# Performance work log

Measured on AMD Instinct MI355X. Metric: run time of the kernel, lower is better.

## Reference

```python
import jax, jax.numpy as jnp
import numpy as np

N_NODES = 100000
N_EDGES = 1600000
D_IN = 128
D_OUT = 128
KEEP_PROB = 0.5  # torch code: p_drop = 1 - self.dropout, dropout=0.5


def setup_inputs() -> dict:
    key = jax.random.key(0)
    k1, k2, k3, k4, k5 = jax.random.split(key, 5)
    x = jax.random.normal(k1, (N_NODES, D_IN), dtype=jnp.float32)
    # Glorot uniform init matching weight_variable_glorot
    init_range = np.sqrt(6.0 / (D_IN + D_OUT))
    W = jax.random.uniform(k2, (D_IN, D_OUT), dtype=jnp.float32,
                           minval=-init_range, maxval=init_range)
    adj_row = jax.random.randint(k3, (N_EDGES,), 0, N_NODES, dtype=jnp.int32)
    adj_col = jax.random.randint(k4, (N_EDGES,), 0, N_NODES, dtype=jnp.int32)
    adj_val = jax.random.uniform(k5, (N_EDGES,), dtype=jnp.float32)
    return {"x": x, "W": W, "adj_row": adj_row, "adj_col": adj_col, "adj_val": adj_val}


def reference(x, W, adj_row, adj_col, adj_val):
    # dropout (always training=True in the torch module), deterministic key
    mask = jax.random.bernoulli(jax.random.key(42), KEEP_PROB, x.shape)
    x = jnp.where(mask, x / KEEP_PROB, 0.0)
    # dense GEMM: [N, D_in] @ [D_in, D_out]
    h = x @ W
    # sparse adjacency SpMM in COO form: out[r] += val * h[c]
    msg = adj_val[:, None] * h[adj_col]            # [E, D_out]
    agg = jax.ops.segment_sum(msg, adj_row, num_segments=N_NODES)
    return jax.nn.relu(agg)
```

## Files before the change

### kernel.cpp

```cpp
#include <hip/hip_runtime.h>
#include <hip/hip_bf16.h>

#define N_NODES 100000
#define N_EDGES 1600000
#define D 128
#define NC 391
#define CCAP 5120
#define NF 3125
#define C1S 32
#define RSS 257
#define GCAP 1024
#define GEMM_H1 1563
#define GEMM_H2 1562

typedef float          floatx4 __attribute__((ext_vector_type(4)));
typedef __bf16         bf16x8  __attribute__((ext_vector_type(8)));
typedef unsigned short ushort8 __attribute__((ext_vector_type(8)));

__device__ __forceinline__ unsigned rotl32(unsigned x, int d) {
    return (x << d) | (x >> (32 - d));
}

__device__ __forceinline__ void threefry_0_42(unsigned c0, unsigned c1,
                                              unsigned& o0, unsigned& o1) {
    const unsigned k0 = 0u, k1 = 42u;
    const unsigned k2 = 0x1BD11BDAu ^ k0 ^ k1;
    unsigned x0 = c0 + k0;
    unsigned x1 = c1 + k1;
#define TF_R4(r0, r1, r2, r3)                      \
    x0 += x1; x1 = rotl32(x1, r0); x1 ^= x0;       \
    x0 += x1; x1 = rotl32(x1, r1); x1 ^= x0;       \
    x0 += x1; x1 = rotl32(x1, r2); x1 ^= x0;       \
    x0 += x1; x1 = rotl32(x1, r3); x1 ^= x0;
    TF_R4(13, 15, 26, 6);  x0 += k1; x1 += k2 + 1u;
    TF_R4(17, 29, 16, 24); x0 += k2; x1 += k0 + 2u;
    TF_R4(13, 15, 26, 6);  x0 += k0; x1 += k1 + 3u;
    TF_R4(17, 29, 16, 24); x0 += k1; x1 += k2 + 4u;
    TF_R4(13, 15, 26, 6);  x0 += k2; x1 += k0 + 5u;
#undef TF_R4
    o0 = x0; o1 = x1;
}

__device__ __forceinline__ bool keep_elem(unsigned i) {
    unsigned o0, o1;
    threefry_0_42(0u, i, o0, o1);
    return (((o0 ^ o1) >> 31) == 0u);
}

__device__ __forceinline__ unsigned short f32_bf16(float f) {
    unsigned u = __float_as_uint(f);
    u += 0x7fffu + ((u >> 16) & 1u);
    return (unsigned short)(u >> 16);
}

__device__ __forceinline__ void gemm_body(const float* __restrict__ x,
                                          const float* __restrict__ W,
                                          unsigned short* __restrict__ hb,
                                          unsigned short (*Wt)[136],
                                          unsigned short (*xs)[136],
                                          int g, int t) {
    {
        int n      = t & 127;
        int k8base = t >> 7;
#pragma unroll
        for (int it = 0; it < 8; ++it) {
            int k8 = (it * 2 + k8base) * 8;
            unsigned short tmp[8];
#pragma unroll
            for (int j = 0; j < 8; ++j)
                tmp[j] = f32_bf16(W[(k8 + j) * 128 + n]);
            *(ushort8*)&Wt[n][k8] = *(ushort8*)tmp;
        }
    }
    {
        int m  = t >> 4;
        int c0 = (t & 15) * 8;
        int r0 = g * 32 + m;
        const float* pa = x + r0 * D + c0;
        const float* pb = x + (r0 + 16) * D + c0;
        float va[8], vb[8];
        *(float4*)&va[0] = ((const float4*)pa)[0];
        *(float4*)&va[4] = ((const float4*)pa)[1];
        *(float4*)&vb[0] = ((const float4*)pb)[0];
        *(float4*)&vb[4] = ((const float4*)pb)[1];
        int ibase = r0 * D + c0;
        unsigned short ta[8], tb[8];
#pragma unroll
        for (int j = 0; j < 8; ++j) {
            float fa = keep_elem((unsigned)(ibase + j))        ? 2.0f * va[j] : 0.0f;
            float fb = keep_elem((unsigned)(ibase + 2048 + j)) ? 2.0f * vb[j] : 0.0f;
            ta[j] = f32_bf16(fa);
            tb[j] = f32_bf16(fb);
        }
        *(ushort8*)&xs[m][c0]      = *(ushort8*)ta;
        *(ushort8*)&xs[16 + m][c0] = *(ushort8*)tb;
    }
    __syncthreads();

    const int w  = t >> 6;
    const int l  = t & 63;
    const int rt = w >> 1;
    const int ctbase = (w & 1) * 4;
    const int mm = l & 15;
    const int q  = l >> 4;
    const int koff = q * 8;
    const unsigned short* xrow = &xs[rt * 16 + mm][0];
    const int growbase = g * 32 + rt * 16;

    for (int ci = 0; ci < 4; ++ci) {
        int ct = ctbase + ci;
        const unsigned short* wrow = &Wt[ct * 16 + mm][0];
        floatx4 acc = {0.f, 0.f, 0.f, 0.f};
#pragma unroll
        for (int kt = 0; kt < 4; ++kt) {
            bf16x8 a = *(const bf16x8*)(xrow + kt * 32 + koff);
            bf16x8 b = *(const bf16x8*)(wrow + kt * 32 + koff);
            acc = __builtin_amdgcn_mfma_f32_16x16x32_bf16(a, b, acc, 0, 0, 0);
        }
        int col = ct * 16 + mm;
#pragma unroll
        for (int reg = 0; reg < 4; ++reg) {
            int grow = growbase + q * 4 + reg;
            hb[grow * D + col] = f32_bf16(acc[reg]);
        }
    }
}

__global__ __launch_bounds__(256)
void k_p1(const float* __restrict__ x, const float* __restrict__ W,
          unsigned short* __restrict__ hb,
          const int* __restrict__ row, const int* __restrict__ col,
          const float* __restrict__ val, int* __restrict__ cnt1,
          int2* __restrict__ buf) {
    __shared__ __align__(16) unsigned short Wt[128][136];
    __shared__ __align__(16) unsigned short xs[32][136];
    __shared__ int h[NC];
    __shared__ int lbase[NC];

    const int t = threadIdx.x;
    if (blockIdx.x >= NC) {
        gemm_body(x, W, hb, Wt, xs, blockIdx.x - NC, t);
        return;
    }

    for (int i = t; i < NC; i += 256) h[i] = 0;
    __syncthreads();

    int rows[16], cols[16];
    float vals[16];
    int base = blockIdx.x * 4096;
#pragma unroll
    for (int k = 0; k < 4; ++k) {
        int e4 = base + (k * 256 + t) * 4;
        if (e4 < N_EDGES) {
            *(int4*)&rows[k * 4]   = *(const int4*)(row + e4);
            *(int4*)&cols[k * 4]   = *(const int4*)(col + e4);
            *(float4*)&vals[k * 4] = *(const float4*)(val + e4);
        } else {
            rows[k * 4] = rows[k * 4 + 1] = rows[k * 4 + 2] = rows[k * 4 + 3] = -1;
        }
    }
#pragma unroll
    for (int j = 0; j < 16; ++j)
        if (rows[j] >= 0) atomicAdd(&h[rows[j] >> 8], 1);
    __syncthreads();

    for (int i = t; i < NC; i += 256) {
        int c = h[i];
        lbase[i] = c ? atomicAdd(&cnt1[i * C1S], c) : 0;
    }
    __syncthreads();
    for (int i = t; i < NC; i += 256) h[i] = 0;
    __syncthreads();

#pragma unroll
    for (int j = 0; j < 16; ++j) {
        if (rows[j] >= 0) {
            int bb  = rows[j] >> 8;
            int pos = lbase[bb] + atomicAdd(&h[bb], 1);
            if (pos < CCAP) {
                int2 ent;
                ent.x = (cols[j] << 7) | ((rows[j] & 255) << 24);
                ent.y = __float_as_int(vals[j]);
                buf[bb * CCAP + pos] = ent;
            }
        }
    }
}

__global__ __launch_bounds__(256)
void k_p2(const float* __restrict__ x, const float* __restrict__ W,
          unsigned short* __restrict__ hb,
          const int* __restrict__ cnt1, int2* __restrict__ buf,
          int* __restrict__ rs) {
    __shared__ __align__(16) unsigned short Wt[128][136];
    __shared__ __align__(16) unsigned short xs[32][136];
    __shared__ int h[4][256];
    __shared__ int wsum[4];

    const int t = threadIdx.x;
    if (blockIdx.x >= NC) {
        gemm_body(x, W, hb, Wt, xs, blockIdx.x - NC + GEMM_H1, t);
        return;
    }

    const int c = blockIdx.x;
    const int w = t >> 6;
    int n = cnt1[c * C1S];
    if (n > CCAP) n = CCAP;
    int2* slab = buf + c * CCAP;

    for (int i = t; i < 1024; i += 256) ((int*)h)[i] = 0;
    __syncthreads();

    int2 er[20];
#pragma unroll
    for (int k = 0; k < 20; ++k) {
        int i = k * 256 + t;
        if (i < n) {
            er[k] = slab[i];
            atomicAdd(&h[w][((unsigned)er[k].x) >> 24], 1);
        }
    }
    __syncthreads();

    int v = h[0][t] + h[1][t] + h[2][t] + h[3][t];
    int xsc = v;
#pragma unroll
    for (int off = 1; off < 64; off <<= 1) {
        int u = __shfl_up(xsc, off);
        if ((t & 63) >= off) xsc += u;
    }
    if ((t & 63) == 63) wsum[t >> 6] = xsc;
    __syncthreads();
    int wo = 0;
    for (int k = 0; k < (t >> 6); ++k) wo += wsum[k];
    int basex = xsc - v + wo;
    rs[c * RSS + t] = basex;
    if (t == 0) rs[c * RSS + 256] = n;
    int s = basex;
#pragma unroll
    for (int wv = 0; wv < 4; ++wv) {
        int tmp = h[wv][t];
        h[wv][t] = s;
        s += tmp;
    }
    __syncthreads();

#pragma unroll
    for (int k = 0; k < 20; ++k) {
        int i = k * 256 + t;
        if (i < n) {
            int pos = atomicAdd(&h[w][((unsigned)er[k].x) >> 24], 1);
            slab[pos] = er[k];
        }
    }
}

__global__ __launch_bounds__(256, 8)
void k_gather(const int* __restrict__ rs, const int2* __restrict__ buf,
              const unsigned short* __restrict__ hb, float* __restrict__ out) {
    __shared__ __align__(16) int2 eL[GCAP];

    const int b = blockIdx.x, t = threadIdx.x;
    const int c = b >> 3;
    const int2* slab = buf + c * CCAP;
    const int* rsb = rs + c * RSS + (b & 7) * 32;
    const int rs0 = rsb[0];
    int nf = rsb[32] - rs0;
    if (nf > GCAP) nf = GCAP;

    for (int i = t; i < nf; i += 256) eL[i] = slab[rs0 + i];
    __syncthreads();

    const int w  = t >> 6;
    const int l2 = (t & 63) * 2;
    const unsigned short* hbl = hb + l2;
    for (int r = 0; r < 8; ++r) {
        int rl = w * 8 + r;
        int s0 = rsb[rl] - rs0;
        int e0 = rsb[rl + 1] - rs0;
        if (e0 > nf) e0 = nf;
        int cc = e0 - s0;
        float a0 = 0.f, a1 = 0.f;
        int i = 0;
        for (; i + 16 <= cc; i += 16) {
            unsigned ex[16];
            float    vv[16];
#pragma unroll
            for (int j = 0; j < 16; ++j) {
                int2 e = eL[s0 + i + j];
                ex[j] = (unsigned)e.x & 0xFFFFFFu;
                vv[j] = __int_as_float(e.y);
            }
            unsigned hv[16];
#pragma unroll
            for (int j = 0; j < 16; ++j)
                hv[j] = *(const unsigned*)(hbl + ex[j]);
#pragma unroll
            for (int j = 0; j < 16; ++j) {
                a0 = fmaf(vv[j], __uint_as_float(hv[j] << 16), a0);
                a1 = fmaf(vv[j], __uint_as_float(hv[j] & 0xffff0000u), a1);
            }
        }
        for (; i + 4 <= cc; i += 4) {
            unsigned ex[4];
            float    vv[4];
#pragma unroll
            for (int j = 0; j < 4; ++j) {
                int2 e = eL[s0 + i + j];
                ex[j] = (unsigned)e.x & 0xFFFFFFu;
                vv[j] = __int_as_float(e.y);
            }
            unsigned hv[4];
#pragma unroll
            for (int j = 0; j < 4; ++j)
                hv[j] = *(const unsigned*)(hbl + ex[j]);
#pragma unroll
            for (int j = 0; j < 4; ++j) {
                a0 = fmaf(vv[j], __uint_as_float(hv[j] << 16), a0);
                a1 = fmaf(vv[j], __uint_as_float(hv[j] & 0xffff0000u), a1);
            }
        }
        for (; i < cc; ++i) {
            int2 e = eL[s0 + i];
            float v = __int_as_float(e.y);
            unsigned hv = *(const unsigned*)(hbl + ((unsigned)e.x & 0xFFFFFFu));
            a0 = fmaf(v, __uint_as_float(hv << 16), a0);
            a1 = fmaf(v, __uint_as_float(hv & 0xffff0000u), a1);
        }
        int grow = (b << 5) + rl;
        float2 rr;
        rr.x = a0 > 0.f ? a0 : 0.f;
        rr.y = a1 > 0.f ? a1 : 0.f;
        *(float2*)(out + grow * D + l2) = rr;
    }
}

extern "C" void kernel_launch(void* const* d_in, const int* in_sizes, int n_in,
                              void* d_out, int out_size, void* d_ws, size_t ws_size,
                              hipStream_t stream) {
    const float* x    = (const float*)d_in[0];
    const float* W    = (const float*)d_in[1];
    const int*   arow = (const int*)d_in[2];
    const int*   acol = (const int*)d_in[3];
    const float* aval = (const float*)d_in[4];
    float* out = (float*)d_out;

    char* ws = (char*)d_ws;
    unsigned short* hb = (unsigned short*)ws;
    size_t off = 25600000;
    int* cnt1 = (int*)(ws + off); off += NC * C1S * 4;
    off = (off + 127) & ~(size_t)127;
    int* rs   = (int*)(ws + off); off += NC * RSS * 4;
    off = (off + 127) & ~(size_t)127;
    int2* buf = (int2*)(ws + off); off += (size_t)NC * CCAP * 8;

    hipMemsetAsync(cnt1, 0, NC * C1S * 4, stream);
    k_p1     <<<NC + GEMM_H1, 256, 0, stream>>>(x, W, hb, arow, acol, aval, cnt1, buf);
    k_p2     <<<NC + GEMM_H2, 256, 0, stream>>>(x, W, hb, cnt1, buf, rs);
    k_gather <<<NF, 256, 0, stream>>>(rs, buf, hb, out);
}
```

Before: 222.5 us.

## Pre-pack W into MFMA fragments, drop per-block W LDS staging, flatten gather loop

A small prep kernel converts W once to bf16 in MFMA fragment order and also zeroes the counters, which replaces the memset. GEMM blocks then load their W fragments straight into registers instead of each block transposing all of W into LDS. This removes a large LDS allocation and redundant per-block conversion work. The gather kernel now walks each wave's whole edge range in one loop and flushes on row-id changes, which avoids per-row loop overhead and uneven unrolling on short rows. Occupancy hints are also changed: 4 for p1/p2, and 8 down to 6 for gather.

```diff
diff --git a/kernel.cpp b/kernel.cpp
--- a/kernel.cpp
+++ b/kernel.cpp
@@ -53,25 +53,37 @@
     return (unsigned short)(u >> 16);
 }
 
+__global__ __launch_bounds__(256)
+void k_wprep(const float* __restrict__ W, unsigned short* __restrict__ Wf,
+             int* __restrict__ cnt1) {
+    int g = blockIdx.x * 256 + threadIdx.x;
+    for (int i = g; i < NC * C1S; i += 2048) cnt1[i] = 0;
+    int combo = g >> 6, l = g & 63;
+    int ct = combo >> 2, kt = combo & 3;
+    int mm = l & 15, q = l >> 4;
+    unsigned short tmp[8];
+#pragma unroll
+    for (int j = 0; j < 8; ++j)
+        tmp[j] = f32_bf16(W[(kt * 32 + q * 8 + j) * 128 + ct * 16 + mm]);
+    *(ushort8*)&Wf[g * 8] = *(ushort8*)tmp;
+}
+
 __device__ __forceinline__ void gemm_body(const float* __restrict__ x,
-                                          const float* __restrict__ W,
+                                          const unsigned short* __restrict__ Wf,
                                           unsigned short* __restrict__ hb,
-                                          unsigned short (*Wt)[136],
                                           unsigned short (*xs)[136],
                                           int g, int t) {
-    {
-        int n      = t & 127;
-        int k8base = t >> 7;
-#pragma unroll
-        for (int it = 0; it < 8; ++it) {
-            int k8 = (it * 2 + k8base) * 8;
-            unsigned short tmp[8];
-#pragma unroll
-            for (int j = 0; j < 8; ++j)
-                tmp[j] = f32_bf16(W[(k8 + j) * 128 + n]);
-            *(ushort8*)&Wt[n][k8] = *(ushort8*)tmp;
-        }
-    }
+    const int w = t >> 6, l = t & 63;
+    const int rt = w >> 1, ctbase = (w & 1) * 4;
+    const int mm = l & 15, q = l >> 4, koff = q * 8;
+
+    bf16x8 wf[4][4];
+#pragma unroll
+    for (int ci = 0; ci < 4; ++ci)
+#pragma unroll
+        for (int kt = 0; kt < 4; ++kt)
+            wf[ci][kt] = *(const bf16x8*)&Wf[(((ctbase + ci) * 4 + kt) * 64 + l) * 8];
+
     {
         int m  = t >> 4;
         int c0 = (t & 15) * 8;
@@ -97,27 +109,20 @@
     }
     __syncthreads();
 
-    const int w  = t >> 6;
-    const int l  = t & 63;
-    const int rt = w >> 1;
-    const int ctbase = (w & 1) * 4;
-    const int mm = l & 15;
-    const int q  = l >> 4;
-    const int koff = q * 8;
     const unsigned short* xrow = &xs[rt * 16 + mm][0];
+    bf16x8 af[4];
+#pragma unroll
+    for (int kt = 0; kt < 4; ++kt)
+        af[kt] = *(const bf16x8*)(xrow + kt * 32 + koff);
+
     const int growbase = g * 32 + rt * 16;
-
+#pragma unroll
     for (int ci = 0; ci < 4; ++ci) {
-        int ct = ctbase + ci;
-        const unsigned short* wrow = &Wt[ct * 16 + mm][0];
         floatx4 acc = {0.f, 0.f, 0.f, 0.f};
 #pragma unroll
-        for (int kt = 0; kt < 4; ++kt) {
-            bf16x8 a = *(const bf16x8*)(xrow + kt * 32 + koff);
-            bf16x8 b = *(const bf16x8*)(wrow + kt * 32 + koff);
-            acc = __builtin_amdgcn_mfma_f32_16x16x32_bf16(a, b, acc, 0, 0, 0);
-        }
-        int col = ct * 16 + mm;
+        for (int kt = 0; kt < 4; ++kt)
+            acc = __builtin_amdgcn_mfma_f32_16x16x32_bf16(af[kt], wf[ci][kt], acc, 0, 0, 0);
+        int col = (ctbase + ci) * 16 + mm;
 #pragma unroll
         for (int reg = 0; reg < 4; ++reg) {
             int grow = growbase + q * 4 + reg;
@@ -126,20 +131,19 @@
     }
 }
 
-__global__ __launch_bounds__(256)
-void k_p1(const float* __restrict__ x, const float* __restrict__ W,
+__global__ __launch_bounds__(256, 4)
+void k_p1(const float* __restrict__ x, const unsigned short* __restrict__ Wf,
           unsigned short* __restrict__ hb,
           const int* __restrict__ row, const int* __restrict__ col,
           const float* __restrict__ val, int* __restrict__ cnt1,
           int2* __restrict__ buf) {
-    __shared__ __align__(16) unsigned short Wt[128][136];
     __shared__ __align__(16) unsigned short xs[32][136];
     __shared__ int h[NC];
     __shared__ int lbase[NC];
 
     const int t = threadIdx.x;
     if (blockIdx.x >= NC) {
-        gemm_body(x, W, hb, Wt, xs, blockIdx.x - NC, t);
+        gemm_body(x, Wf, hb, xs, blockIdx.x - NC, t);
         return;
     }
 
@@ -188,19 +192,18 @@
     }
 }
 
-__global__ __launch_bounds__(256)
-void k_p2(const float* __restrict__ x, const float* __restrict__ W,
+__global__ __launch_bounds__(256, 4)
+void k_p2(const float* __restrict__ x, const unsigned short* __restrict__ Wf,
           unsigned short* __restrict__ hb,
           const int* __restrict__ cnt1, int2* __restrict__ buf,
           int* __restrict__ rs) {
-    __shared__ __align__(16) unsigned short Wt[128][136];
     __shared__ __align__(16) unsigned short xs[32][136];
     __shared__ int h[4][256];
     __shared__ int wsum[4];
 
     const int t = threadIdx.x;
     if (blockIdx.x >= NC) {
-        gemm_body(x, W, hb, Wt, xs, blockIdx.x - NC + GEMM_H1, t);
+        gemm_body(x, Wf, hb, xs, blockIdx.x - NC + GEMM_H1, t);
         return;
     }
 
@@ -257,7 +260,7 @@
     }
 }
 
-__global__ __launch_bounds__(256, 8)
+__global__ __launch_bounds__(256, 6)
 void k_gather(const int* __restrict__ rs, const int2* __restrict__ buf,
               const unsigned short* __restrict__ hb, float* __restrict__ out) {
     __shared__ __align__(16) int2 eL[GCAP];
@@ -276,65 +279,76 @@
     const int w  = t >> 6;
     const int l2 = (t & 63) * 2;
     const unsigned short* hbl = hb + l2;
-    for (int r = 0; r < 8; ++r) {
-        int rl = w * 8 + r;
-        int s0 = rsb[rl] - rs0;
-        int e0 = rsb[rl + 1] - rs0;
-        if (e0 > nf) e0 = nf;
-        int cc = e0 - s0;
-        float a0 = 0.f, a1 = 0.f;
-        int i = 0;
-        for (; i + 16 <= cc; i += 16) {
-            unsigned ex[16];
-            float    vv[16];
-#pragma unroll
-            for (int j = 0; j < 16; ++j) {
-                int2 e = eL[s0 + i + j];
-                ex[j] = (unsigned)e.x & 0xFFFFFFu;
-                vv[j] = __int_as_float(e.y);
-            }
-            unsigned hv[16];
-#pragma unroll
-            for (int j = 0; j < 16; ++j)
-                hv[j] = *(const unsigned*)(hbl + ex[j]);
-#pragma unroll
-            for (int j = 0; j < 16; ++j) {
-                a0 = fmaf(vv[j], __uint_as_float(hv[j] << 16), a0);
-                a1 = fmaf(vv[j], __uint_as_float(hv[j] & 0xffff0000u), a1);
-            }
-        }
-        for (; i + 4 <= cc; i += 4) {
-            unsigned ex[4];
-            float    vv[4];
-#pragma unroll
-            for (int j = 0; j < 4; ++j) {
-                int2 e = eL[s0 + i + j];
-                ex[j] = (unsigned)e.x & 0xFFFFFFu;
-                vv[j] = __int_as_float(e.y);
-            }
-            unsigned hv[4];
-#pragma unroll
-            for (int j = 0; j < 4; ++j)
-                hv[j] = *(const unsigned*)(hbl + ex[j]);
-#pragma unroll
-            for (int j = 0; j < 4; ++j) {
-                a0 = fmaf(vv[j], __uint_as_float(hv[j] << 16), a0);
-                a1 = fmaf(vv[j], __uint_as_float(hv[j] & 0xffff0000u), a1);
-            }
-        }
-        for (; i < cc; ++i) {
-            int2 e = eL[s0 + i];
-            float v = __int_as_float(e.y);
-            unsigned hv = *(const unsigned*)(hbl + ((unsigned)e.x & 0xFFFFFFu));
-            a0 = fmaf(v, __uint_as_float(hv << 16), a0);
-            a1 = fmaf(v, __uint_as_float(hv & 0xffff0000u), a1);
-        }
-        int grow = (b << 5) + rl;
-        float2 rr;
-        rr.x = a0 > 0.f ? a0 : 0.f;
-        rr.y = a1 > 0.f ? a1 : 0.f;
-        *(float2*)(out + grow * D + l2) = rr;
-    }
+
+    int s0w = rsb[w * 8] - rs0;     if (s0w > nf) s0w = nf;
+    int e0w = rsb[w * 8 + 8] - rs0; if (e0w > nf) e0w = nf;
+
+    float a0 = 0.f, a1 = 0.f;
+    int cur = w * 8;
+    const int wtop = w * 8 + 8;
+
+#define STORE_ROW(R, X0, X1)                                      \
+    {                                                             \
+        float2 rr;                                                \
+        rr.x = (X0) > 0.f ? (X0) : 0.f;                           \
+        rr.y = (X1) > 0.f ? (X1) : 0.f;                           \
+        *(float2*)(out + ((b << 5) + (R)) * D + l2) = rr;         \
+    }
+#define FLUSH(RID)                                                \
+    if ((RID) != cur) {                                           \
+        STORE_ROW(cur, a0, a1);                                   \
+        for (int z = cur + 1; z < (RID); ++z) STORE_ROW(z, 0.f, 0.f); \
+        a0 = 0.f; a1 = 0.f; cur = (RID);                          \
+    }
+
+    int i = s0w;
+    for (; i + 16 <= e0w; i += 16) {
+        int2 e[16];
+#pragma unroll
+        for (int j = 0; j < 16; ++j) e[j] = eL[i + j];
+        unsigned hv[16];
+#pragma unroll
+        for (int j = 0; j < 16; ++j)
+            hv[j] = *(const unsigned*)(hbl + ((unsigned)e[j].x & 0xFFFFFFu));
+#pragma unroll
+        for (int j = 0; j < 16; ++j) {
+            int rid = ((unsigned)e[j].x >> 24) & 31;
+            FLUSH(rid);
+            float v = __int_as_float(e[j].y);
+            a0 = fmaf(v, __uint_as_float(hv[j] << 16), a0);
+            a1 = fmaf(v, __uint_as_float(hv[j] & 0xffff0000u), a1);
+        }
+    }
+    for (; i + 4 <= e0w; i += 4) {
+        int2 e[4];
+#pragma unroll
+        for (int j = 0; j < 4; ++j) e[j] = eL[i + j];
+        unsigned hv[4];
+#pragma unroll
+        for (int j = 0; j < 4; ++j)
+            hv[j] = *(const unsigned*)(hbl + ((unsigned)e[j].x & 0xFFFFFFu));
+#pragma unroll
+        for (int j = 0; j < 4; ++j) {
+            int rid = ((unsigned)e[j].x >> 24) & 31;
+            FLUSH(rid);
+            float v = __int_as_float(e[j].y);
+            a0 = fmaf(v, __uint_as_float(hv[j] << 16), a0);
+            a1 = fmaf(v, __uint_as_float(hv[j] & 0xffff0000u), a1);
+        }
+    }
+    for (; i < e0w; ++i) {
+        int2 e = eL[i];
+        unsigned hv = *(const unsigned*)(hbl + ((unsigned)e.x & 0xFFFFFFu));
+        int rid = ((unsigned)e.x >> 24) & 31;
+        FLUSH(rid);
+        float v = __int_as_float(e.y);
+        a0 = fmaf(v, __uint_as_float(hv << 16), a0);
+        a1 = fmaf(v, __uint_as_float(hv & 0xffff0000u), a1);
+    }
+    STORE_ROW(cur, a0, a1);
+    for (int z = cur + 1; z < wtop; ++z) STORE_ROW(z, 0.f, 0.f);
+#undef FLUSH
+#undef STORE_ROW
 }
 
 extern "C" void kernel_launch(void* const* d_in, const int* in_sizes, int n_in,
@@ -352,12 +366,14 @@
     size_t off = 25600000;
     int* cnt1 = (int*)(ws + off); off += NC * C1S * 4;
     off = (off + 127) & ~(size_t)127;
+    unsigned short* Wf = (unsigned short*)(ws + off); off += 32768;
+    off = (off + 127) & ~(size_t)127;
     int* rs   = (int*)(ws + off); off += NC * RSS * 4;
     off = (off + 127) & ~(size_t)127;
     int2* buf = (int2*)(ws + off); off += (size_t)NC * CCAP * 8;
 
-    hipMemsetAsync(cnt1, 0, NC * C1S * 4, stream);
-    k_p1     <<<NC + GEMM_H1, 256, 0, stream>>>(x, W, hb, arow, acol, aval, cnt1, buf);
-    k_p2     <<<NC + GEMM_H2, 256, 0, stream>>>(x, W, hb, cnt1, buf, rs);
+    k_wprep  <<<8, 256, 0, stream>>>(W, Wf, cnt1);
+    k_p1     <<<NC + GEMM_H1, 256, 0, stream>>>(x, Wf, hb, arow, acol, aval, cnt1, buf);
+    k_p2     <<<NC + GEMM_H2, 256, 0, stream>>>(x, Wf, hb, cnt1, buf, rs);
     k_gather <<<NF, 256, 0, stream>>>(rs, buf, hb, out);
 }
```

Measured after the change: 228.5 us. +2.7%, slower.
